# Performance work log

Measured on AMD Instinct MI355X. Metric: run time of the kernel, lower is better.

The kernel has to match this reference:

```python
import math
import jax, jax.numpy as jnp
import numpy as np

B, CIN, COUT, K, S = 2, 64, 64, 3, 18  # batch, channels, kernel size per dim, spatial size per dim


def setup_inputs() -> dict:
    key = jax.random.key(0)
    k1, k2 = jax.random.split(key)
    inputs = jax.random.normal(k1, (B, CIN, S, S, S, S), dtype=jnp.float32)
    std = 1.0 / math.sqrt(CIN * K ** 4)  # matches init_weight: 1/sqrt(in_channels * n_offsets)
    kernel = jax.random.uniform(k2, (K ** 4, CIN, COUT), dtype=jnp.float32, minval=-std, maxval=std)
    return {"inputs": inputs, "kernel": kernel}


def reference(inputs, kernel):
    # kernel: [k0*k1*k2*k3, Cin, Cout], offsets enumerated row-major over the 4 kernel dims.
    # Equivalent to the per-offset matmul + shift-accumulate in conv4d (valid padding,
    # stride=1, dilation=1), expressed as a single 4-spatial-dim XLA convolution.
    cin, cout = kernel.shape[1], kernel.shape[2]
    w = kernel.reshape(K, K, K, K, cin, cout).transpose(5, 4, 0, 1, 2, 3)  # OIWXYZ
    out = jax.lax.conv_general_dilated(
        inputs, w,
        window_strides=(1, 1, 1, 1),
        padding='VALID',
        rhs_dilation=(1, 1, 1, 1),
        dimension_numbers=('NCWXYZ', 'OIWXYZ', 'NCWXYZ'),
    )  # [B, Cout, 16, 16, 16, 16]
    return out
```

## Files before the change

kernel.cpp:

```cpp
#include <hip/hip_runtime.h>


typedef __attribute__((ext_vector_type(8))) short bf16x8;
typedef __attribute__((ext_vector_type(4))) float f32x4;
typedef __attribute__((ext_vector_type(8))) unsigned short ushort8;
typedef unsigned short u16;
typedef unsigned int u32;

#define S_OFF_BYTES 663552u
#define WS_NEEDED   27537408u

__device__ __forceinline__ u16 f2bf(float f) {
    u32 u = __float_as_uint(f);
    u += 0x7FFFu + ((u >> 16) & 1u);
    return (u16)(u >> 16);
}

__global__ __launch_bounds__(256) void wprep(const float* __restrict__ ker, u16* __restrict__ wg) {
    const int g = blockIdx.x * 256 + threadIdx.x;
    const int l = g & 63, ks = (g >> 6) & 1, rt = (g >> 7) & 3, off = g >> 9;
    const int co  = rt * 16 + (l & 15);
    const int ci0 = ks * 32 + (l >> 4) * 8;
    const float* p = ker + (size_t)off * 4096 + co;
    ushort8 v;
#pragma unroll
    for (int e = 0; e < 8; ++e) v[e] = f2bf(p[(size_t)(ci0 + e) * 64]);
    *(ushort8*)(wg + (size_t)g * 8) = v;
}

__global__ __launch_bounds__(256) void sprep(const float* __restrict__ in, u16* __restrict__ s) {
    __shared__ u16 L[64 * 330];
    const int blk = blockIdx.x;
    const int b = blk / 324, wx = blk - b * 324;
    const float* src = in + (size_t)b * 6718464 + (wx / 18) * 5832 + (wx % 18) * 324;
    const int t = threadIdx.x;
    for (int i = t; i < 5184; i += 256) {
        const int ci = i / 81, j = i - ci * 81;
        float4 v = *(const float4*)(src + (size_t)ci * 104976 + j * 4);
        u32* q = (u32*)&L[ci * 330 + j * 4];
        q[0] = f2bf(v.x) | ((u32)f2bf(v.y) << 16);
        q[1] = f2bf(v.z) | ((u32)f2bf(v.w) << 16);
    }
    __syncthreads();
    u16* dst = s + (size_t)blk * 20736;
    for (int i = t; i < 2592; i += 256) {
        const int ks = i / 1296, r4 = i - ks * 1296;
        const int rem = r4 >> 2, g = r4 & 3;
        ushort8 v;
#pragma unroll
        for (int e = 0; e < 8; ++e) v[e] = L[(ks * 32 + g * 8 + e) * 330 + rem];
        const int gp = g ^ ((rem >> 1) & 3);
        *(ushort8*)(dst + ks * 10368 + rem * 32 + gp * 8) = v;
    }
}

__global__ __launch_bounds__(256, 2)
void conv4d_main(const u16* __restrict__ wg, const u16* __restrict__ s, float* __restrict__ out) {
    __shared__ u16 R[3][324 * 32];

    const int bid = blockIdx.x;
    const int bs  = (bid & 7) * 64 + (bid >> 3);
    const int b   = bs >> 8;
    const int w   = (bs >> 4) & 15;
    const int x   = bs & 15;

    const int t  = threadIdx.x, wv = t >> 6, l = t & 63;
    const int lg = l >> 4, ll = l & 15;

    f32x4 acc[4][4];
#pragma unroll
    for (int i = 0; i < 4; ++i)
#pragma unroll
        for (int j = 0; j < 4; ++j) acc[i][j] = (f32x4){0.f, 0.f, 0.f, 0.f};

    const u16* sb = s + (size_t)(b * 324 + w * 18 + x) * 20736;

#define STAGE_U(h, slot)                                                                 \
    do {                                                                                 \
        const int kwx_ = (h) >> 1, ks_ = (h) & 1;                                        \
        const int kw_ = kwx_ / 3, kx_ = kwx_ - kw_ * 3;                                  \
        const u16* src_ = sb + (size_t)(kw_ * 18 + kx_) * 20736 + ks_ * 10368;           \
        const int base_ = wv * 324;                                                      \
        _Pragma("unroll")                                                                \
        for (int k_ = 0; k_ < 5; ++k_) {                                                 \
            const int i_ = base_ + k_ * 64 + l;                                          \
            __builtin_amdgcn_global_load_lds(                                            \
                (const __attribute__((address_space(1))) u32*)(src_ + (size_t)i_ * 8),   \
                (__attribute__((address_space(3))) u32*)&R[slot][i_ * 8], 16, 0, 0);     \
        }                                                                                \
        if (l < 4) {                                                                     \
            const int i_ = base_ + 320 + l;                                              \
            __builtin_amdgcn_global_load_lds(                                            \
                (const __attribute__((address_space(1))) u32*)(src_ + (size_t)i_ * 8),   \
                (__attribute__((address_space(3))) u32*)&R[slot][i_ * 8], 16, 0, 0);     \
        }                                                                                \
    } while (0)

    STAGE_U(0, 0);
    STAGE_U(1, 1);
    asm volatile("s_waitcnt vmcnt(6)" ::: "memory");
    __builtin_amdgcn_sched_barrier(0);
    __builtin_amdgcn_s_barrier();

    for (int p = 0; p < 18; ++p) {
        if (p + 2 < 18) STAGE_U(p + 2, (p + 2) % 3);

        const int kwx = p >> 1, ks = p & 1;
        const u16* wo = wg + (size_t)(kwx * 9) * 4096 + ks * 512;
        const u16* Tb = R[p % 3];

        bf16x8 a[4][4];
#pragma unroll
        for (int i = 0; i < 3; ++i)
#pragma unroll
            for (int rt = 0; rt < 4; ++rt)
                a[i][rt] = *(const bf16x8*)(wo + (size_t)i * 4096 + (size_t)rt * 1024 + l * 8);

#pragma unroll
        for (int sub = 0; sub < 9; ++sub) {
            if (sub + 3 < 9) {
                const u16* wn = wo + (size_t)(sub + 3) * 4096;
#pragma unroll
                for (int rt = 0; rt < 4; ++rt)
                    a[(sub + 3) & 3][rt] = *(const bf16x8*)(wn + (size_t)rt * 1024 + l * 8);
            }
            const int ky = sub / 3, kz = sub - ky * 3;
            bf16x8 bfr[4];
#pragma unroll
            for (int ct = 0; ct < 4; ++ct) {
                const int rem = (4 * wv + ct + ky) * 18 + ll + kz;
                bfr[ct] = *(const bf16x8*)&Tb[rem * 32 + ((lg ^ ((rem >> 1) & 3)) << 3)];
            }
            __builtin_amdgcn_s_setprio(1);
#pragma unroll
            for (int ct = 0; ct < 4; ++ct)
#pragma unroll
                for (int rt = 0; rt < 4; ++rt)
                    acc[rt][ct] = __builtin_amdgcn_mfma_f32_16x16x32_bf16(
                        a[sub & 3][rt], bfr[ct], acc[rt][ct], 0, 0, 0);
            __builtin_amdgcn_s_setprio(0);
        }

        if (p < 17) {
            if (p < 16) asm volatile("s_waitcnt vmcnt(6)" ::: "memory");
            else        asm volatile("s_waitcnt vmcnt(0)" ::: "memory");
            __builtin_amdgcn_sched_barrier(0);
            __builtin_amdgcn_s_barrier();
        }
    }
#undef STAGE_U

    float* ob = out + (size_t)b * 4194304 + (size_t)w * 4096 + (size_t)x * 256;
#pragma unroll
    for (int rt = 0; rt < 4; ++rt) {
        const int co0 = rt * 16 + 4 * lg;
#pragma unroll
        for (int ct = 0; ct < 4; ++ct) {
            const int base = (4 * wv + ct) * 16 + ll;
#pragma unroll
            for (int r = 0; r < 4; ++r)
                ob[(size_t)(co0 + r) * 65536 + base] = acc[rt][ct][r];
        }
    }
}

__global__ __launch_bounds__(512, 2)
void conv4d_mfma(const float* __restrict__ in, const float* __restrict__ ker,
                 float* __restrict__ out) {
    __shared__ unsigned short T[18 * 18 * 64];
    __shared__ unsigned short Wt[2][64 * 64];
    const int bx = blockIdx.x;
    const int b = bx >> 8, wsp = (bx >> 4) & 15, x = bx & 15;
    const int t = threadIdx.x, wv = t >> 6, l = t & 63;
    const int lg = l >> 4, ll = l & 15;
    const float* inb = in + (size_t)b * 6718464 + wsp * 5832 + x * 324;
    f32x4 acc[4][2];
#pragma unroll
    for (int i = 0; i < 4; ++i)
#pragma unroll
        for (int j = 0; j < 2; ++j) acc[i][j] = (f32x4){0.f, 0.f, 0.f, 0.f};
#pragma unroll
    for (int f0 = 0; f0 < 4096; f0 += 512) {
        const int f = f0 + t, ci = f >> 6, co = f & 63;
        Wt[0][co * 64 + ((((ci >> 3) ^ (co & 7)) << 3) | (ci & 7))] = f2bf(ker[f]);
    }
    for (int off = 0; off < 81; ++off) {
        const int sub = off % 9;
        if (sub == 0) {
            const int kw = off / 27, kx = (off / 9) % 3;
            const float* p = inb + kw * 5832 + kx * 324;
            for (int f = t; f < 18 * 18 * 64; f += 512) {
                const int ci = f / 324, rem = f - ci * 324, zp = rem % 18;
                T[rem * 64 + ((((ci >> 3) ^ (zp & 7)) << 3) | (ci & 7))] =
                    f2bf(p[(size_t)ci * 104976 + rem]);
            }
        }
        if (off + 1 < 81) {
            const float* p = ker + (off + 1) * 4096;
            unsigned short* wb = Wt[(off + 1) & 1];
#pragma unroll
            for (int f0 = 0; f0 < 4096; f0 += 512) {
                const int f = f0 + t, ci = f >> 6, co = f & 63;
                wb[co * 64 + ((((ci >> 3) ^ (co & 7)) << 3) | (ci & 7))] = f2bf(p[f]);
            }
        }
        if (sub == 0) __syncthreads();
        const int ky = sub / 3, kz = sub - ky * 3;
        const int zp = ll + kz, zs = zp & 7;
#pragma unroll
        for (int ks = 0; ks < 2; ++ks) {
            bf16x8 af[4];
#pragma unroll
            for (int rt = 0; rt < 4; ++rt)
                af[rt] = *(const bf16x8*)&Wt[off & 1][(rt * 16 + ll) * 64 + (((lg + 4 * ks) ^ (ll & 7)) << 3)];
#pragma unroll
            for (int ct = 0; ct < 2; ++ct) {
                const int rem = (2 * wv + ct + ky) * 18 + zp;
                const bf16x8 bfr = *(const bf16x8*)&T[rem * 64 + (((lg + 4 * ks) ^ zs) << 3)];
#pragma unroll
                for (int rt = 0; rt < 4; ++rt)
                    acc[rt][ct] = __builtin_amdgcn_mfma_f32_16x16x32_bf16(af[rt], bfr, acc[rt][ct], 0, 0, 0);
            }
        }
        __syncthreads();
    }
    float* ob = out + (size_t)b * 4194304 + wsp * 4096 + x * 256;
#pragma unroll
    for (int rt = 0; rt < 4; ++rt) {
        const int co0 = rt * 16 + 4 * lg;
#pragma unroll
        for (int ct = 0; ct < 2; ++ct) {
            const int base = (2 * wv + ct) * 16 + ll;
#pragma unroll
            for (int r = 0; r < 4; ++r)
                ob[(size_t)(co0 + r) * 65536 + base] = acc[rt][ct][r];
        }
    }
}

extern "C" void kernel_launch(void* const* d_in, const int* in_sizes, int n_in,
                              void* d_out, int out_size, void* d_ws, size_t ws_size,
                              hipStream_t stream) {
    const float* in  = (const float*)d_in[0];
    const float* ker = (const float*)d_in[1];
    float* out = (float*)d_out;
    if (ws_size >= (size_t)WS_NEEDED) {
        u16* wg = (u16*)d_ws;
        u16* s  = (u16*)((char*)d_ws + S_OFF_BYTES);
        wprep<<<dim3(162), dim3(256), 0, stream>>>(ker, wg);
        sprep<<<dim3(648), dim3(256), 0, stream>>>(in, s);
        conv4d_main<<<dim3(512), dim3(256), 0, stream>>>(wg, s, out);
    } else {
        conv4d_mfma<<<dim3(512), dim3(512), 0, stream>>>(in, ker, out);
    }
}
```

Before: 100.9 us.

## Reuse LDS B fragments across ky and prefetch weights across phases

Reorders the 9 sub-iterations to go kz-major, so each wave loads 6 B fragments per kz into two register banks and reuses them across the three ky shifts. This replaces 4 LDS reads per sub-iteration with 6 reads per kz. Weight A-fragments are now kept in a 3-deep rotating register buffer that prefetches across phase boundaries instead of reloading at each phase start. The explicit vmcnt waits plus s_barrier are replaced by __syncthreads, which may drain outstanding global_load_lds prefetches sooner and reduce the overlap of staging with compute.

```diff
diff --git a/kernel.cpp b/kernel.cpp
--- a/kernel.cpp
+++ b/kernel.cpp
@@ -98,55 +98,64 @@
 
     STAGE_U(0, 0);
     STAGE_U(1, 1);
-    asm volatile("s_waitcnt vmcnt(6)" ::: "memory");
-    __builtin_amdgcn_sched_barrier(0);
-    __builtin_amdgcn_s_barrier();
+
+    bf16x8 a[3][4];
+#pragma unroll
+    for (int i = 0; i < 3; ++i)
+#pragma unroll
+        for (int rt = 0; rt < 4; ++rt)
+            a[i][rt] = *(const bf16x8*)(wg + (size_t)(i * 3) * 4096 + (size_t)rt * 1024 + l * 8);
+
+    __syncthreads();
+
+    bf16x8 bb[2][6];
 
     for (int p = 0; p < 18; ++p) {
         if (p + 2 < 18) STAGE_U(p + 2, (p + 2) % 3);
 
-        const int kwx = p >> 1, ks = p & 1;
-        const u16* wo = wg + (size_t)(kwx * 9) * 4096 + ks * 512;
         const u16* Tb = R[p % 3];
 
-        bf16x8 a[4][4];
-#pragma unroll
-        for (int i = 0; i < 3; ++i)
-#pragma unroll
-            for (int rt = 0; rt < 4; ++rt)
-                a[i][rt] = *(const bf16x8*)(wo + (size_t)i * 4096 + (size_t)rt * 1024 + l * 8);
-
-#pragma unroll
-        for (int sub = 0; sub < 9; ++sub) {
-            if (sub + 3 < 9) {
-                const u16* wn = wo + (size_t)(sub + 3) * 4096;
-#pragma unroll
-                for (int rt = 0; rt < 4; ++rt)
-                    a[(sub + 3) & 3][rt] = *(const bf16x8*)(wn + (size_t)rt * 1024 + l * 8);
-            }
-            const int ky = sub / 3, kz = sub - ky * 3;
-            bf16x8 bfr[4];
-#pragma unroll
-            for (int ct = 0; ct < 4; ++ct) {
-                const int rem = (4 * wv + ct + ky) * 18 + ll + kz;
-                bfr[ct] = *(const bf16x8*)&Tb[rem * 32 + ((lg ^ ((rem >> 1) & 3)) << 3)];
-            }
+#define LOADB(bank, kz_)                                                             \
+        do {                                                                         \
+            _Pragma("unroll")                                                        \
+            for (int q_ = 0; q_ < 6; ++q_) {                                         \
+                const int rem_ = (4 * wv + q_) * 18 + ll + (kz_);                    \
+                bb[bank][q_] = *(const bf16x8*)&Tb[rem_ * 32 +                       \
+                                   ((lg ^ ((rem_ >> 1) & 3)) << 3)];                 \
+            }                                                                        \
+        } while (0)
+
+#pragma unroll
+        for (int j = 0; j < 9; ++j) {
+            const int ky = j % 3;
+            if (j == 0) LOADB(0, 0);
+            if (j == 1) LOADB(1, 1);
+            if (j == 3) LOADB(0, 2);
+            const int bank = (j >= 3 && j < 6) ? 1 : 0;
+
             __builtin_amdgcn_s_setprio(1);
 #pragma unroll
             for (int ct = 0; ct < 4; ++ct)
 #pragma unroll
                 for (int rt = 0; rt < 4; ++rt)
                     acc[rt][ct] = __builtin_amdgcn_mfma_f32_16x16x32_bf16(
-                        a[sub & 3][rt], bfr[ct], acc[rt][ct], 0, 0, 0);
+                        a[j % 3][rt], bb[bank][ct + ky], acc[rt][ct], 0, 0, 0);
             __builtin_amdgcn_s_setprio(0);
-        }
-
-        if (p < 17) {
-            if (p < 16) asm volatile("s_waitcnt vmcnt(6)" ::: "memory");
-            else        asm volatile("s_waitcnt vmcnt(0)" ::: "memory");
-            __builtin_amdgcn_sched_barrier(0);
-            __builtin_amdgcn_s_barrier();
-        }
+
+            {
+                const int pj = (j + 3 < 9) ? p : p + 1;
+                const int jj = (j + 3) % 9;
+                if (pj < 18) {
+                    const int sub2 = (jj % 3) * 3 + jj / 3;
+                    const u16* wn = wg + (size_t)((pj >> 1) * 9 + sub2) * 4096 + (pj & 1) * 512;
+#pragma unroll
+                    for (int rt = 0; rt < 4; ++rt)
+                        a[j % 3][rt] = *(const bf16x8*)(wn + (size_t)rt * 1024 + l * 8);
+                }
+            }
+        }
+#undef LOADB
+        __syncthreads();
     }
 #undef STAGE_U
 
```

New measurement: 92.43 us. -8.4%, faster.

## Stage weights in LDS per kz phase and reuse B fragments across ky

Applied to the files above, without the earlier changes.

Weight fragments are now staged into LDS through async global-to-LDS loads, one slot per kz phase, instead of being read per wave straight from global memory. The activation tile buffer shrinks from triple to double buffering. Each kz phase loads six B fragments once and reuses them across the three ky offsets, cutting LDS reads from twelve to six per phase. The price is a more intricate wait/barrier schedule with three barriers per p iteration, and exact vmcnt counts that must match the issued loads.

```diff
diff --git a/kernel.cpp b/kernel.cpp
--- a/kernel.cpp
+++ b/kernel.cpp
@@ -56,7 +56,8 @@
 
 __global__ __launch_bounds__(256, 2)
 void conv4d_main(const u16* __restrict__ wg, const u16* __restrict__ s, float* __restrict__ out) {
-    __shared__ u16 R[3][324 * 32];
+    __shared__ u16 A[3][6144];
+    __shared__ u16 Bq[2][10368];
 
     const int bid = blockIdx.x;
     const int bs  = (bid & 7) * 64 + (bid >> 3);
@@ -75,7 +76,21 @@
 
     const u16* sb = s + (size_t)(b * 324 + w * 18 + x) * 20736;
 
-#define STAGE_U(h, slot)                                                                 \
+#define STAGE_A(p2, kz2, slot)                                                           \
+    do {                                                                                 \
+        const int kwx_ = (p2) >> 1, ks2_ = (p2) & 1;                                     \
+        _Pragma("unroll")                                                                \
+        for (int c_ = 0; c_ < 3; ++c_) {                                                 \
+            const u16* src_ = wg + (size_t)(kwx_ * 9 + c_ * 3 + (kz2)) * 4096            \
+                              + wv * 1024 + ks2_ * 512 + l * 8;                          \
+            __builtin_amdgcn_global_load_lds(                                            \
+                (const __attribute__((address_space(1))) u32*)src_,                      \
+                (__attribute__((address_space(3))) u32*)&A[slot][c_ * 2048 + wv * 512 + l * 8], \
+                16, 0, 0);                                                               \
+        }                                                                                \
+    } while (0)
+
+#define STAGE_B(h)                                                                       \
     do {                                                                                 \
         const int kwx_ = (h) >> 1, ks_ = (h) & 1;                                        \
         const int kw_ = kwx_ / 3, kx_ = kwx_ - kw_ * 3;                                  \
@@ -86,69 +101,77 @@
             const int i_ = base_ + k_ * 64 + l;                                          \
             __builtin_amdgcn_global_load_lds(                                            \
                 (const __attribute__((address_space(1))) u32*)(src_ + (size_t)i_ * 8),   \
-                (__attribute__((address_space(3))) u32*)&R[slot][i_ * 8], 16, 0, 0);     \
+                (__attribute__((address_space(3))) u32*)&Bq[(h) & 1][i_ * 8], 16, 0, 0); \
         }                                                                                \
         if (l < 4) {                                                                     \
             const int i_ = base_ + 320 + l;                                              \
             __builtin_amdgcn_global_load_lds(                                            \
                 (const __attribute__((address_space(1))) u32*)(src_ + (size_t)i_ * 8),   \
-                (__attribute__((address_space(3))) u32*)&R[slot][i_ * 8], 16, 0, 0);     \
-        }                                                                                \
-    } while (0)
-
-    STAGE_U(0, 0);
-    STAGE_U(1, 1);
-    asm volatile("s_waitcnt vmcnt(6)" ::: "memory");
-    __builtin_amdgcn_sched_barrier(0);
-    __builtin_amdgcn_s_barrier();
+                (__attribute__((address_space(3))) u32*)&Bq[(h) & 1][i_ * 8], 16, 0, 0); \
+        }                                                                                \
+    } while (0)
+
+#define PHASE_COMPUTE(qc, Tb)                                                            \
+    do {                                                                                 \
+        bf16x8 af[3][4];                                                                 \
+        bf16x8 bb[6];                                                                    \
+        _Pragma("unroll")                                                                \
+        for (int ky_ = 0; ky_ < 3; ++ky_)                                                \
+            _Pragma("unroll")                                                            \
+            for (int rt_ = 0; rt_ < 4; ++rt_)                                            \
+                af[ky_][rt_] = *(const bf16x8*)&A[qc][ky_ * 2048 + rt_ * 512 + l * 8];   \
+        _Pragma("unroll")                                                                \
+        for (int q_ = 0; q_ < 6; ++q_) {                                                 \
+            const int rem_ = (4 * wv + q_) * 18 + ll + (qc);                             \
+            bb[q_] = *(const bf16x8*)&(Tb)[rem_ * 32 + ((lg ^ ((rem_ >> 1) & 3)) << 3)]; \
+        }                                                                                \
+        __builtin_amdgcn_s_setprio(1);                                                   \
+        _Pragma("unroll")                                                                \
+        for (int ky_ = 0; ky_ < 3; ++ky_)                                                \
+            _Pragma("unroll")                                                            \
+            for (int ct_ = 0; ct_ < 4; ++ct_)                                            \
+                _Pragma("unroll")                                                        \
+                for (int rt_ = 0; rt_ < 4; ++rt_)                                        \
+                    acc[rt_][ct_] = __builtin_amdgcn_mfma_f32_16x16x32_bf16(             \
+                        af[ky_][rt_], bb[ct_ + ky_], acc[rt_][ct_], 0, 0, 0);            \
+        __builtin_amdgcn_s_setprio(0);                                                   \
+    } while (0)
+
+#define WAITBAR(N)                                                                       \
+    do {                                                                                 \
+        asm volatile("s_waitcnt vmcnt(" #N ")" ::: "memory");                            \
+        __builtin_amdgcn_sched_barrier(0);                                               \
+        __builtin_amdgcn_s_barrier();                                                    \
+    } while (0)
+
+    STAGE_A(0, 0, 0);
+    STAGE_A(0, 1, 1);
+    STAGE_B(0);
+    WAITBAR(0);
 
     for (int p = 0; p < 18; ++p) {
-        if (p + 2 < 18) STAGE_U(p + 2, (p + 2) % 3);
-
-        const int kwx = p >> 1, ks = p & 1;
-        const u16* wo = wg + (size_t)(kwx * 9) * 4096 + ks * 512;
-        const u16* Tb = R[p % 3];
-
-        bf16x8 a[4][4];
-#pragma unroll
-        for (int i = 0; i < 3; ++i)
-#pragma unroll
-            for (int rt = 0; rt < 4; ++rt)
-                a[i][rt] = *(const bf16x8*)(wo + (size_t)i * 4096 + (size_t)rt * 1024 + l * 8);
-
-#pragma unroll
-        for (int sub = 0; sub < 9; ++sub) {
-            if (sub + 3 < 9) {
-                const u16* wn = wo + (size_t)(sub + 3) * 4096;
-#pragma unroll
-                for (int rt = 0; rt < 4; ++rt)
-                    a[(sub + 3) & 3][rt] = *(const bf16x8*)(wn + (size_t)rt * 1024 + l * 8);
-            }
-            const int ky = sub / 3, kz = sub - ky * 3;
-            bf16x8 bfr[4];
-#pragma unroll
-            for (int ct = 0; ct < 4; ++ct) {
-                const int rem = (4 * wv + ct + ky) * 18 + ll + kz;
-                bfr[ct] = *(const bf16x8*)&Tb[rem * 32 + ((lg ^ ((rem >> 1) & 3)) << 3)];
-            }
-            __builtin_amdgcn_s_setprio(1);
-#pragma unroll
-            for (int ct = 0; ct < 4; ++ct)
-#pragma unroll
-                for (int rt = 0; rt < 4; ++rt)
-                    acc[rt][ct] = __builtin_amdgcn_mfma_f32_16x16x32_bf16(
-                        a[sub & 3][rt], bfr[ct], acc[rt][ct], 0, 0, 0);
-            __builtin_amdgcn_s_setprio(0);
-        }
+        const u16* Tb = Bq[p & 1];
+
+        STAGE_A(p, 2, 2);
+        PHASE_COMPUTE(0, Tb);
+        WAITBAR(3);
 
         if (p < 17) {
-            if (p < 16) asm volatile("s_waitcnt vmcnt(6)" ::: "memory");
-            else        asm volatile("s_waitcnt vmcnt(0)" ::: "memory");
-            __builtin_amdgcn_sched_barrier(0);
-            __builtin_amdgcn_s_barrier();
-        }
-    }
-#undef STAGE_U
+            STAGE_A(p + 1, 0, 0);
+            STAGE_B(p + 1);
+        }
+        PHASE_COMPUTE(1, Tb);
+        if (p < 17) WAITBAR(9);
+        else        WAITBAR(0);
+
+        if (p < 17) STAGE_A(p + 1, 1, 1);
+        PHASE_COMPUTE(2, Tb);
+        if (p < 17) WAITBAR(3);
+    }
+#undef STAGE_A
+#undef STAGE_B
+#undef PHASE_COMPUTE
+#undef WAITBAR
 
     float* ob = out + (size_t)b * 4194304 + (size_t)w * 4096 + (size_t)x * 256;
 #pragma unroll
```

After: 93.26 us. 1.08x faster.
